# Kernel tuning notes

Measured on AMD Instinct MI355X. Metric: run time of the kernel, lower is better.

The kernel has to match this reference:

```python
import jax, jax.numpy as jnp
import numpy as np

B, L, D = 2, 2048, 1024
H, K = 16, 16
HD = D // H


def setup_inputs() -> dict:
    key = jax.random.key(0)
    k1, k2, k3, k4, k5 = jax.random.split(key, 5)
    x = jax.random.normal(k1, (B, L, D), dtype=jnp.float32)
    # Linear weight (out_features, in_features), small init to keep logits sane
    w_in = jax.random.normal(k2, (3 * D, D), dtype=jnp.float32) * 0.02
    # TISA radial-basis kernel parameters, per (head, kernel)
    kernel_offsets = jax.random.normal(k3, (H, K), dtype=jnp.float32) * 20.0
    kernel_amplitudes = 0.1 + 0.01 * jax.random.normal(k4, (H, K), dtype=jnp.float32)
    kernel_sharpness = 0.1 + 0.01 * jax.random.normal(k5, (H, K), dtype=jnp.float32)
    return {"x": x, "w_in": w_in, "kernel_offsets": kernel_offsets,
            "kernel_amplitudes": kernel_amplitudes, "kernel_sharpness": kernel_sharpness}


def tisa_bias(offsets, amplitudes, sharpness, seq_len):
    # relative positions -(L-1) .. (L-1)  -> per-head RBF positional scores
    rel = jnp.arange(-(seq_len - 1), seq_len, dtype=jnp.float32)  # (2L-1,)
    # scores[h, m] = sum_k amp[h,k] * exp(-|sharp[h,k]| * (off[h,k] - rel[m])^2)
    diff = offsets[:, :, None] - rel[None, None, :]               # (H, K, 2L-1)
    scores = jnp.sum(amplitudes[:, :, None] * jnp.exp(-jnp.abs(sharpness)[:, :, None] * diff * diff), axis=1)  # (H, 2L-1)
    # Toeplitz expansion: bias[h, i, j] = scores[h, (i - j) + (L-1)]
    i = jnp.arange(seq_len)
    idx = i[:, None] - i[None, :] + (seq_len - 1)                 # (L, L)
    return scores[:, idx]                                         # (H, L, L)


def reference(x, w_in, kernel_offsets, kernel_amplitudes, kernel_sharpness):
    b, l, d = x.shape
    proj = jnp.einsum('bld,ed->ble', x, w_in)                     # (B, L, 3D)
    # split: memory = first 2D (k then v), query = last D
    k_, v_, q_ = proj[..., :d], proj[..., d:2 * d], proj[..., 2 * d:]

    def heads(t):
        return t.reshape(b, l, H, HD).transpose(0, 2, 1, 3)       # (B, H, L, HD)

    q, k, v = heads(q_), heads(k_), heads(v_)
    bias = tisa_bias(kernel_offsets, kernel_amplitudes, kernel_sharpness, l)  # (H, L, L)
    scale = 1.0 / np.sqrt(HD).astype(np.float32)
    logits = jnp.einsum('bhld,bhmd->bhlm', q, k) * scale + bias[None]
    attn = jax.nn.softmax(logits, axis=-1)
    out = jnp.einsum('bhlm,bhmd->bhld', attn, v)                  # (B, H, L, HD)
    return out.transpose(0, 2, 1, 3).reshape(b, l, d)             # (B, L, D)
```

## Files before the change

### kernel.cpp

```cpp
#include <hip/hip_runtime.h>
#include <hip/hip_bf16.h>
#include <stdint.h>
#include <stddef.h>


#define NB     2
#define NH     16
#define SL     2048
#define DH     64
#define DMODEL 1024
#define SCP    4096
#define CTS    136

typedef __attribute__((ext_vector_type(8)))  short bf16x8;
typedef __attribute__((ext_vector_type(4)))  short bf16x4;
typedef __attribute__((ext_vector_type(4)))  float f32x4;
typedef __attribute__((ext_vector_type(16))) float f32x16;

static __device__ __forceinline__ short f2bf(float x) {
  __hip_bfloat16 h = __float2bfloat16(x);
  return *reinterpret_cast<short*>(&h);
}
static __device__ __forceinline__ long long bf4_to_ll(bf16x4 v) {
  long long r; __builtin_memcpy(&r, &v, 8); return r;
}
static __device__ __forceinline__ bf16x4 ll_to_bf4(long long v) {
  bf16x4 r; __builtin_memcpy(&r, &v, 8); return r;
}
#define GLD(g, l) __builtin_amdgcn_global_load_lds( \
    (const __attribute__((address_space(1))) void*)(g), \
    (__attribute__((address_space(3))) void*)(l), 16, 0, 0)

__global__ __launch_bounds__(256) void prep_k(
    const float* __restrict__ x, const float* __restrict__ w,
    const float* __restrict__ koff, const float* __restrict__ kamp,
    const float* __restrict__ kshp,
    short* __restrict__ xbf, short* __restrict__ wbf,
    float* __restrict__ scores) {
  const int bx = blockIdx.x, tid = threadIdx.x;
  if (bx < 7168) {
    const float* src = (bx < 4096) ? x : w;
    short* dst       = (bx < 4096) ? xbf : wbf;
    const int i      = (bx < 4096 ? bx : bx - 4096) * 256 + tid;
    float4 a = *(const float4*)(src + (size_t)i * 4);
    bf16x4 o;
    o.x = f2bf(a.x); o.y = f2bf(a.y); o.z = f2bf(a.z); o.w = f2bf(a.w);
    *(bf16x4*)(dst + (size_t)i * 4) = o;
  } else {
    const int idx = bx - 7168;
    const int h = idx >> 4;
    const int r = (idx & 15) * 256 + tid;
    if (r >= 4095) return;
    float rel = (float)(r - (SL - 1));
    float acc = 0.f;
#pragma unroll
    for (int k = 0; k < 16; ++k) {
      float o = koff[h * 16 + k];
      float a = kamp[h * 16 + k];
      float s = fabsf(kshp[h * 16 + k]);
      float d = o - rel;
      acc += a * __expf(-s * d * d);
    }
    scores[h * SCP + r] = acc;
  }
}

__global__ __launch_bounds__(256) void qkv_gemm_k(
    const short* __restrict__ A, const short* __restrict__ Bw,
    __hip_bfloat16* __restrict__ kbuf, __hip_bfloat16* __restrict__ vbufT,
    __hip_bfloat16* __restrict__ qbuf) {
  __shared__ __align__(16) short SM[128 * CTS];
  short* As = SM;
  short* Bs = SM + 128 * 64;
  const int tid  = threadIdx.x;
  const int lane = tid & 63;
  const int wv   = tid >> 6;
  const int l15  = lane & 15, quad = lane >> 4;
  const int wm = (wv & 1) * 64, wn = (wv >> 1) * 64;
  const int m0 = blockIdx.y * 128, n0 = blockIdx.x * 128;
  const int which = n0 >> 10;

  f32x4 acc[4][4];
#pragma unroll
  for (int r = 0; r < 4; ++r)
#pragma unroll
    for (int c = 0; c < 4; ++c) acc[r][c] = (f32x4){0.f, 0.f, 0.f, 0.f};

  for (int kt = 0; kt < 16; ++kt) {
    const int k0 = kt * 64;
#pragma unroll
    for (int it = 0; it < 4; ++it) {
      const int e8  = it * 256 + tid;
      const int row = e8 >> 3;
      const int col = (e8 & 7) * 8;
      GLD(A + (size_t)(m0 + row) * DMODEL + k0 + col, &As[e8 * 8]);
      GLD(Bw + (size_t)(n0 + row) * DMODEL + k0 + col, &Bs[e8 * 8]);
    }
    __syncthreads();
#pragma unroll
    for (int ki = 0; ki < 64; ki += 32) {
      bf16x8 af[4], bfv[4];
#pragma unroll
      for (int r = 0; r < 4; ++r)
        af[r] = *(const bf16x8*)&As[(wm + r * 16 + l15) * 64 + ki + quad * 8];
#pragma unroll
      for (int c = 0; c < 4; ++c)
        bfv[c] = *(const bf16x8*)&Bs[(wn + c * 16 + l15) * 64 + ki + quad * 8];
#pragma unroll
      for (int r = 0; r < 4; ++r)
#pragma unroll
        for (int c = 0; c < 4; ++c)
          acc[r][c] = __builtin_amdgcn_mfma_f32_16x16x32_bf16(af[r], bfv[c], acc[r][c], 0, 0, 0);
    }
    __syncthreads();
  }

  const int bb  = m0 >> 11;
  const int llb = m0 & 2047;
  const int hhb = (n0 >> 6) & 15;
  if (which != 1) {
    const float qs = (which == 2) ? 0.125f : 1.0f;
#pragma unroll
    for (int r = 0; r < 4; ++r)
#pragma unroll
      for (int c = 0; c < 4; ++c)
#pragma unroll
        for (int g = 0; g < 4; ++g)
          SM[(wm + r * 16 + quad * 4 + g) * CTS + wn + c * 16 + l15] =
              f2bf(acc[r][c][g] * qs);
    __syncthreads();
    __hip_bfloat16* dst = (which == 0) ? kbuf : qbuf;
#pragma unroll
    for (int i = 0; i < 8; ++i) {
      const int cidx = i * 256 + tid;
      const int m = cidx >> 4, ch = cidx & 15;
      bf16x8 val = *(const bf16x8*)&SM[m * CTS + ch * 8];
      const int hh  = hhb + (ch >> 3);
      const int hd0 = (ch & 7) * 8;
      *(bf16x8*)&dst[(((size_t)bb * NH + hh) * SL + llb + m) * DH + hd0] = val;
    }
  } else {
#pragma unroll
    for (int r = 0; r < 4; ++r)
#pragma unroll
      for (int c = 0; c < 4; ++c) {
        bf16x4 pk;
#pragma unroll
        for (int g = 0; g < 4; ++g) pk[g] = f2bf(acc[r][c][g]);
        *(bf16x4*)&SM[(wn + c * 16 + l15) * CTS + wm + r * 16 + quad * 4] = pk;
      }
    __syncthreads();
#pragma unroll
    for (int i = 0; i < 8; ++i) {
      const int cidx = i * 256 + tid;
      const int n = cidx >> 4, ch = cidx & 15;
      bf16x8 val = *(const bf16x8*)&SM[n * CTS + ch * 8];
      const int hh = hhb + (n >> 6);
      const int hd = n & 63;
      *(bf16x8*)&vbufT[(((size_t)bb * NH + hh) * DH + hd) * SL + llb + ch * 8] = val;
    }
  }
}

__global__ __launch_bounds__(128, 2) void attn_k(
    const __hip_bfloat16* __restrict__ qbuf, const __hip_bfloat16* __restrict__ kbuf,
    const __hip_bfloat16* __restrict__ vbufT, const float* __restrict__ scores,
    float* __restrict__ out) {
  __shared__ __align__(16) short Ks[64 * 72];
  __shared__ __align__(16) short Vs[64 * 72];
  __shared__ __align__(16) float Bss[2112];
  const int bh   = blockIdx.x;
  const int b    = bh >> 4, h = bh & 15;
  const int tid  = threadIdx.x;
  const int lane = tid & 63;
  const int wv   = tid >> 6;
  const int n32  = lane & 31, hf = lane >> 5;
  const int i0b  = blockIdx.y * 64;
  const int i0   = i0b + wv * 32;
  const __hip_bfloat16* qb = qbuf + (size_t)bh * SL * DH;
  const short* kb = (const short*)(kbuf + (size_t)bh * SL * DH);
  const short* vb = (const short*)(vbufT + (size_t)bh * DH * SL);
  const float* sc = scores + h * SCP;

  {
    const float* bsrc = sc + i0b;
#pragma unroll
    for (int i = 0; i < 4; ++i)
      GLD(bsrc + (size_t)(i * 128 + tid) * 4, &Bss[(i * 128 + tid) * 4]);
    if (tid < 16) GLD(bsrc + (size_t)(512 + tid) * 4, &Bss[(512 + tid) * 4]);
  }

  bf16x8 qf[4];
#pragma unroll
  for (int kc = 0; kc < 4; ++kc)
    qf[kc] = *(const bf16x8*)&qb[(size_t)(i0 + n32) * DH + kc * 16 + hf * 8];

  f32x16 ot[2];
#pragma unroll
  for (int dt = 0; dt < 2; ++dt)
#pragma unroll
    for (int r = 0; r < 16; ++r) ot[dt][r] = 0.f;
  float lsum = 0.f;

  for (int j0 = 0; j0 < SL; j0 += 64) {
    {
      const short* ksrc = kb + (size_t)j0 * DH;
#pragma unroll
      for (int i = 0; i < 4; ++i) {
        int c = i * 128 + tid; int r = c / 9, s = c - r * 9;
        GLD(ksrc + (size_t)r * DH + s * 8, &Ks[c * 8]);
      }
      if (tid < 64) {
        int c = 512 + tid; int r = c / 9, s = c - r * 9;
        GLD(ksrc + (size_t)r * DH + s * 8, &Ks[c * 8]);
      }
    }
    {
#pragma unroll
      for (int i = 0; i < 4; ++i) {
        int c = i * 128 + tid; int r = c / 9, s = c - r * 9;
        GLD(vb + (size_t)r * SL + j0 + s * 8, &Vs[c * 8]);
      }
      if (tid < 64) {
        int c = 512 + tid; int r = c / 9, s = c - r * 9;
        GLD(vb + (size_t)r * SL + j0 + s * 8, &Vs[c * 8]);
      }
    }
    __syncthreads();

#pragma unroll
    for (int kt = 0; kt < 2; ++kt) {
      f32x16 st;
#pragma unroll
      for (int r = 0; r < 16; ++r) st[r] = 0.f;
#pragma unroll
      for (int kc = 0; kc < 4; ++kc) {
        bf16x8 kf = *(const bf16x8*)&Ks[(kt * 32 + n32) * 72 + kc * 16 + hf * 8];
        st = __builtin_amdgcn_mfma_f32_32x32x16_bf16(kf, qf[kc], st, 0, 0, 0);
      }
      bf16x4 pk[4];
      const int tb0 = wv * 32 + n32 - j0 - kt * 32 - 4 * hf + 2047;
#pragma unroll
      for (int g = 0; g < 4; ++g) {
        const int tb = tb0 - 8 * g;
#pragma unroll
        for (int i = 0; i < 4; ++i) {
          const float p = __expf(st[g * 4 + i] + Bss[tb - i]);
          lsum += p;
          pk[g][i] = f2bf(p);
        }
      }
      long long s0 = hf ? bf4_to_ll(pk[0]) : bf4_to_ll(pk[1]);
      bf16x4 r0 = ll_to_bf4(__shfl_xor(s0, 32));
      bf16x8 pf0 = hf == 0 ? __builtin_shufflevector(pk[0], r0, 0, 1, 2, 3, 4, 5, 6, 7)
                           : __builtin_shufflevector(r0, pk[1], 0, 1, 2, 3, 4, 5, 6, 7);
      long long s1 = hf ? bf4_to_ll(pk[2]) : bf4_to_ll(pk[3]);
      bf16x4 r1 = ll_to_bf4(__shfl_xor(s1, 32));
      bf16x8 pf1 = hf == 0 ? __builtin_shufflevector(pk[2], r1, 0, 1, 2, 3, 4, 5, 6, 7)
                           : __builtin_shufflevector(r1, pk[3], 0, 1, 2, 3, 4, 5, 6, 7);
#pragma unroll
      for (int dt = 0; dt < 2; ++dt) {
        const short* vr = &Vs[(dt * 32 + n32) * 72 + kt * 32];
        bf16x8 vf0 = *(const bf16x8*)&vr[hf * 8];
        bf16x8 vf1 = *(const bf16x8*)&vr[16 + hf * 8];
        ot[dt] = __builtin_amdgcn_mfma_f32_32x32x16_bf16(vf0, pf0, ot[dt], 0, 0, 0);
        ot[dt] = __builtin_amdgcn_mfma_f32_32x32x16_bf16(vf1, pf1, ot[dt], 0, 0, 0);
      }
    }
    __syncthreads();
  }

  lsum += __shfl_xor(lsum, 32);
  const float inv = 1.f / lsum;
  float* orow = out + (((size_t)b * SL + i0 + n32) * NH + h) * DH;
#pragma unroll
  for (int dt = 0; dt < 2; ++dt)
#pragma unroll
    for (int g = 0; g < 4; ++g) {
      f32x4 v;
#pragma unroll
      for (int i = 0; i < 4; ++i) v[i] = ot[dt][g * 4 + i] * inv;
      *(f32x4*)&orow[dt * 32 + 8 * g + 4 * hf] = v;
    }
}

extern "C" void kernel_launch(void* const* d_in, const int* in_sizes, int n_in,
                              void* d_out, int out_size, void* d_ws, size_t ws_size,
                              hipStream_t stream) {
  const float* x    = (const float*)d_in[0];
  const float* w    = (const float*)d_in[1];
  const float* koff = (const float*)d_in[2];
  const float* kamp = (const float*)d_in[3];
  const float* kshp = (const float*)d_in[4];
  float* out = (float*)d_out;

  const size_t per = (size_t)NB * NH * SL * DH;
  const size_t nx  = (size_t)NB * SL * DMODEL;
  const size_t nw  = (size_t)3 * DMODEL * DMODEL;

  __hip_bfloat16* kbuf  = (__hip_bfloat16*)d_ws;
  __hip_bfloat16* vbufT = kbuf + per;
  __hip_bfloat16* qbuf  = vbufT + per;
  float* scores = (float*)(qbuf + per);
  short* xbf    = (short*)(scores + (size_t)NH * SCP);
  short* wbf    = xbf + nx;

  prep_k<<<7424, 256, 0, stream>>>(x, w, koff, kamp, kshp, xbf, wbf, scores);
  qkv_gemm_k<<<dim3(24, 32), 256, 0, stream>>>(xbf, wbf, kbuf, vbufT, qbuf);
  attn_k<<<dim3(NB * NH, SL / 64), 128, 0, stream>>>(qbuf, kbuf, vbufT, scores, out);
}
```

Measured before the change: 197.3 us.

## Remap GEMM blocks per XCD, add fast bf16 rounding, hoist load index math

The QKV GEMM now launches as a 1D grid and remaps block IDs so that consecutive blocks on the same XCD share row tiles, which should improve L2 reuse of the A operand. A truncating round-half-up float-to-bf16 conversion replaces the library conversion in the GEMM epilogue and in the attention probability packing. In the attention kernel, the divide-by-9 load indices are computed once before the loop instead of on every tile. The fast conversion does not handle NaN and does not round ties to even, which changes rounding slightly.

```diff
diff --git a/kernel.cpp b/kernel.cpp
--- a/kernel.cpp
+++ b/kernel.cpp
@@ -20,6 +20,10 @@
 static __device__ __forceinline__ short f2bf(float x) {
   __hip_bfloat16 h = __float2bfloat16(x);
   return *reinterpret_cast<short*>(&h);
+}
+static __device__ __forceinline__ short f2bf_fast(float x) {
+  union { float f; uint32_t u; } v; v.f = x;
+  return (short)((v.u + 0x8000u) >> 16);
 }
 static __device__ __forceinline__ long long bf4_to_ll(bf16x4 v) {
   long long r; __builtin_memcpy(&r, &v, 8); return r;
@@ -77,7 +81,11 @@
   const int wv   = tid >> 6;
   const int l15  = lane & 15, quad = lane >> 4;
   const int wm = (wv & 1) * 64, wn = (wv >> 1) * 64;
-  const int m0 = blockIdx.y * 128, n0 = blockIdx.x * 128;
+  const int bid = blockIdx.x;
+  const int xcd = bid & 7, g = bid >> 3;
+  const int xt  = g % 24;
+  const int yt  = (g / 24) * 8 + xcd;
+  const int m0 = yt * 128, n0 = xt * 128;
   const int which = n0 >> 10;
 
   f32x4 acc[4][4];
@@ -125,9 +133,9 @@
 #pragma unroll
       for (int c = 0; c < 4; ++c)
 #pragma unroll
-        for (int g = 0; g < 4; ++g)
-          SM[(wm + r * 16 + quad * 4 + g) * CTS + wn + c * 16 + l15] =
-              f2bf(acc[r][c][g] * qs);
+        for (int gg = 0; gg < 4; ++gg)
+          SM[(wm + r * 16 + quad * 4 + gg) * CTS + wn + c * 16 + l15] =
+              f2bf_fast(acc[r][c][gg] * qs);
     __syncthreads();
     __hip_bfloat16* dst = (which == 0) ? kbuf : qbuf;
 #pragma unroll
@@ -146,7 +154,7 @@
       for (int c = 0; c < 4; ++c) {
         bf16x4 pk;
 #pragma unroll
-        for (int g = 0; g < 4; ++g) pk[g] = f2bf(acc[r][c][g]);
+        for (int gg = 0; gg < 4; ++gg) pk[gg] = f2bf_fast(acc[r][c][gg]);
         *(bf16x4*)&SM[(wn + c * 16 + l15) * CTS + wm + r * 16 + quad * 4] = pk;
       }
     __syncthreads();
@@ -190,6 +198,13 @@
     if (tid < 16) GLD(bsrc + (size_t)(512 + tid) * 4, &Bss[(512 + tid) * 4]);
   }
 
+  int rc[5], scnk[5];
+#pragma unroll
+  for (int i = 0; i < 5; ++i) {
+    const int c = i * 128 + tid;
+    rc[i] = c / 9; scnk[i] = (c - rc[i] * 9) * 8;
+  }
+
   bf16x8 qf[4];
 #pragma unroll
   for (int kc = 0; kc < 4; ++kc)
@@ -203,29 +218,15 @@
   float lsum = 0.f;
 
   for (int j0 = 0; j0 < SL; j0 += 64) {
-    {
-      const short* ksrc = kb + (size_t)j0 * DH;
-#pragma unroll
-      for (int i = 0; i < 4; ++i) {
-        int c = i * 128 + tid; int r = c / 9, s = c - r * 9;
-        GLD(ksrc + (size_t)r * DH + s * 8, &Ks[c * 8]);
-      }
-      if (tid < 64) {
-        int c = 512 + tid; int r = c / 9, s = c - r * 9;
-        GLD(ksrc + (size_t)r * DH + s * 8, &Ks[c * 8]);
-      }
-    }
-    {
-#pragma unroll
-      for (int i = 0; i < 4; ++i) {
-        int c = i * 128 + tid; int r = c / 9, s = c - r * 9;
-        GLD(vb + (size_t)r * SL + j0 + s * 8, &Vs[c * 8]);
-      }
-      if (tid < 64) {
-        int c = 512 + tid; int r = c / 9, s = c - r * 9;
-        GLD(vb + (size_t)r * SL + j0 + s * 8, &Vs[c * 8]);
-      }
-    }
+    const short* ksrc = kb + (size_t)j0 * DH;
+#pragma unroll
+    for (int i = 0; i < 4; ++i)
+      GLD(ksrc + (size_t)rc[i] * DH + scnk[i], &Ks[(i * 128 + tid) * 8]);
+    if (tid < 64) GLD(ksrc + (size_t)rc[4] * DH + scnk[4], &Ks[(512 + tid) * 8]);
+#pragma unroll
+    for (int i = 0; i < 4; ++i)
+      GLD(vb + (size_t)rc[i] * SL + j0 + scnk[i], &Vs[(i * 128 + tid) * 8]);
+    if (tid < 64) GLD(vb + (size_t)rc[4] * SL + j0 + scnk[4], &Vs[(512 + tid) * 8]);
     __syncthreads();
 
 #pragma unroll
@@ -247,7 +248,7 @@
         for (int i = 0; i < 4; ++i) {
           const float p = __expf(st[g * 4 + i] + Bss[tb - i]);
           lsum += p;
-          pk[g][i] = f2bf(p);
+          pk[g][i] = f2bf_fast(p);
         }
       }
       long long s0 = hf ? bf4_to_ll(pk[0]) : bf4_to_ll(pk[1]);
@@ -306,6 +307,6 @@
   short* wbf    = xbf + nx;
 
   prep_k<<<7424, 256, 0, stream>>>(x, w, koff, kamp, kshp, xbf, wbf, scores);
-  qkv_gemm_k<<<dim3(24, 32), 256, 0, stream>>>(xbf, wbf, kbuf, vbufT, qbuf);
+  qkv_gemm_k<<<768, 256, 0, stream>>>(xbf, wbf, kbuf, vbufT, qbuf);
   attn_k<<<dim3(NB * NH, SL / 64), 128, 0, stream>>>(qbuf, kbuf, vbufT, scores, out);
 }
```

After: 202.4 us. 2.6% more time.
